# Kernel optimization log

Measured on AMD Instinct MI355X. Metric: run time of the kernel, lower is better.

The kernel has to match this reference:

```python
import jax, jax.numpy as jnp
import numpy as np

WINDOW = 60
DEPTH = 3
HIDDEN = 256
LN_EPS = 1e-5


def _lyndon_indices(d):
    # Lyndon words over alphabet {0..d-1}, lengths 2 and 3, lexicographic order
    # (signatory mode='words' extracts expanded-logsig coefficients at Lyndon words).
    i2 = np.array([(i, j) for i in range(d) for j in range(d) if (i, j) < (j, i)], dtype=np.int32)
    i3 = np.array([(i, j, k) for i in range(d) for j in range(d) for k in range(d)
                   if (i, j, k) < (j, k, i) and (i, j, k) < (k, i, j)], dtype=np.int32)
    return i2, i3


def _logsig_features(x):
    # x: [b, s, c] -> logsignature of time-augmented sliding windows: [b*s, sig_channels]
    b, s, c = x.shape
    d = c + 1
    # replicate-padded sliding windows via clipped gather (matches F.pad replicate + unfold)
    pos = jnp.clip(jnp.arange(s)[:, None] + jnp.arange(WINDOW)[None, :] - (WINDOW - 1), 0, s - 1)
    windows = x[:, pos, :]                                   # [b, s, W, c]
    t = jnp.linspace(0.0, 1.0, WINDOW, dtype=x.dtype)        # time augmentation channel
    t_b = jnp.broadcast_to(t[None, None, :, None], (b, s, WINDOW, 1))
    aug = jnp.concatenate([t_b, windows], axis=-1).reshape(b * s, WINDOW, d)
    N = b * s
    # basepoint=True: prepend zero point -> increments include the first point itself
    inc = jnp.diff(aug, axis=1, prepend=jnp.zeros((N, 1, d), aug.dtype))  # [N, W, d]
    inc_t = jnp.transpose(inc, (1, 0, 2))                    # [W, N, d]

    def chen_step(carry, v):
        S1, S2, S3 = carry
        vv = jnp.einsum('ni,nj->nij', v, v)
        vvv = jnp.einsum('nij,nk->nijk', vv, v)
        nS3 = S3 + jnp.einsum('nij,nk->nijk', S2, v) \
                 + 0.5 * jnp.einsum('ni,njk->nijk', S1, vv) + vvv / 6.0
        nS2 = S2 + jnp.einsum('ni,nj->nij', S1, v) + 0.5 * vv
        nS1 = S1 + v
        return (nS1, nS2, nS3), None

    init = (jnp.zeros((N, d), x.dtype), jnp.zeros((N, d, d), x.dtype), jnp.zeros((N, d, d, d), x.dtype))
    (S1, S2, S3), _ = jax.lax.scan(chen_step, init, inc_t)
    # log in truncated tensor algebra: log(1+x) = x - x^2/2 + x^3/3
    L1 = S1
    L2 = S2 - 0.5 * jnp.einsum('ni,nj->nij', S1, S1)
    L3 = (S3 - 0.5 * (jnp.einsum('ni,njk->nijk', S1, S2) + jnp.einsum('nij,nk->nijk', S2, S1))
          + jnp.einsum('ni,nj,nk->nijk', S1, S1, S1) / 3.0)
    i2, i3 = _lyndon_indices(d)
    f2 = L2[:, i2[:, 0], i2[:, 1]]
    f3 = L3[:, i3[:, 0], i3[:, 1], i3[:, 2]]
    return jnp.concatenate([L1, f2, f3], axis=-1)            # [N, sig_channels]


def setup_inputs() -> dict:
    key = jax.random.key(0)
    ks = jax.random.split(key, 5)
    b, s, c = 8, 2048, 8
    d = c + 1
    sig_channels = d + (d * d - d) // 2 + (d ** 3 - d) // 3  # 285 for d=9
    h2 = 2 * HIDDEN
    x = jax.random.normal(ks[0], (b, s, c), dtype=jnp.float32)
    w1 = jax.random.normal(ks[1], (sig_channels, h2), dtype=jnp.float32) / np.sqrt(sig_channels)
    b1 = jnp.zeros((h2,), jnp.float32)
    ln_g = jnp.ones((h2,), jnp.float32)
    ln_b = jnp.zeros((h2,), jnp.float32)
    w2 = jax.random.normal(ks[2], (h2, HIDDEN), dtype=jnp.float32) / np.sqrt(h2)
    b2 = jnp.zeros((HIDDEN,), jnp.float32)
    return {"x": x, "w1": w1, "b1": b1, "ln_g": ln_g, "ln_b": ln_b, "w2": w2, "b2": b2}


def reference(x, w1, b1, ln_g, ln_b, w2, b2):
    b, s, _ = x.shape
    feats = _logsig_features(x)                              # [b*s, sig_channels]
    h = jax.nn.gelu(feats @ w1 + b1, approximate=False)      # torch default GELU (erf)
    mu = jnp.mean(h, axis=-1, keepdims=True)
    var = jnp.var(h, axis=-1, keepdims=True)
    h = (h - mu) / jnp.sqrt(var + LN_EPS) * ln_g + ln_b      # LayerNorm; Dropout is eval no-op
    out = h @ w2 + b2
    return out.reshape(b, s, -1)
```

## Files before the change

kernel.cpp:

```cpp
#include <hip/hip_runtime.h>
#include <hip/hip_bf16.h>
#include <cstdint>
#include <cstddef>

typedef short short8 __attribute__((ext_vector_type(8)));
typedef float f32x4 __attribute__((ext_vector_type(4)));
typedef float f32x2 __attribute__((ext_vector_type(2)));

#define NS    2048
#define KPAD  288
#define H2    512
#define HID   256
#define WPB   7
#define SBLK  293

#define MFMA(a,b,c) __builtin_amdgcn_mfma_f32_16x16x32_bf16((a),(b),(c),0,0,0)

__device__ __forceinline__ void gl2lds16(const void* g, void* l) {
    __builtin_amdgcn_global_load_lds(
        (const __attribute__((address_space(1))) void*)g,
        (__attribute__((address_space(3))) void*)l, 16, 0, 0);
}
__device__ __forceinline__ float geluf(float x) {
    return 0.5f * x * (1.0f + erff(x * 0.70710678118654752f));
}
__device__ __forceinline__ f32x4 shfl4(f32x4 v, int d) {
    f32x4 r;
    r[0] = __shfl_xor(v[0], d); r[1] = __shfl_xor(v[1], d);
    r[2] = __shfl_xor(v[2], d); r[3] = __shfl_xor(v[3], d);
    return r;
}

struct Tbl3 { short col[729]; };
static constexpr Tbl3 make_tbl3() {
    Tbl3 t{};
    for (int x = 0; x < 729; ++x) t.col[x] = -1;
    int r = 0;
    for (int i = 0; i < 9; ++i)
        for (int j = 0; j < 9; ++j)
            for (int k = 0; k < 9; ++k) {
                bool lt1 = (i < j) || (i == j && (j < k || (j == k && k < i)));
                bool lt2 = (i < k) || (i == k && (j < i || (j == i && k < j)));
                if (lt1 && lt2) { t.col[(i*9+j)*9+k] = (short)(45 + r); ++r; }
            }
    return t;
}
static constexpr Tbl3 TBL3 = make_tbl3();

#define SIG_STEP(VA_,VB_,VC_) { \
    const float hh = 0.5f * S1i + vi * (1.0f/6.0f); \
    const float ra = S2ra + hh * (VA_); \
    const float rb = S2rb + hh * (VB_); \
    const float rc = S2rc + hh * (VC_); \
    const f32x2 ra2 = {ra, ra}, rb2 = {rb, rb}, rc2 = {rc, rc}; \
    S3sa += ra * v0; S3pa0 += ra2*vp0; S3pa1 += ra2*vp1; S3pa2 += ra2*vp2; S3pa3 += ra2*vp3; \
    S3sb += rb * v0; S3pb0 += rb2*vp0; S3pb1 += rb2*vp1; S3pb2 += rb2*vp2; S3pb3 += rb2*vp3; \
    S3sc += rc * v0; S3pc0 += rc2*vp0; S3pc1 += rc2*vp1; S3pc2 += rc2*vp2; S3pc3 += rc2*vp3; \
    const float aa = S1i + 0.5f * vi; \
    S2ra += aa * (VA_); S2rb += aa * (VB_); S2rc += aa * (VC_); \
    S1i += vi; }

#define SIG_MAIN(VA_,VB_,VC_) { \
    { const float* xr = &X[(g0 - lo) * 8]; \
      const float4 e0 = *(const float4*)xr; \
      const float4 e1 = *(const float4*)(xr + 4); \
      const float rs = xr[ioff]; \
      const float v0 = 0.0f; \
      const f32x2 vp0 = {e0.x, e0.y}, vp1 = {e0.z, e0.w}, vp2 = {e1.x, e1.y}, vp3 = {e1.z, e1.w}; \
      const float vi = (ci == 0) ? 0.0f : rs; \
      SIG_STEP(VA_,VB_,VC_) } \
    const float* pd = &PD[(sm59 + 1 - lo + 59) * 8]; \
    float4 d0 = *(const float4*)pd; \
    float4 d1 = *(const float4*)(pd + 4); \
    float rn = pd[ioff]; \
    _Pragma("unroll 2") \
    for (int j = 1; j < 60; ++j) { \
      const float4 e0 = d0; const float4 e1 = d1; const float rs = rn; \
      pd += 8; \
      d0 = *(const float4*)pd; d1 = *(const float4*)(pd + 4); rn = pd[ioff]; \
      const float v0 = DT; \
      const f32x2 vp0 = {e0.x, e0.y}, vp1 = {e0.z, e0.w}, vp2 = {e1.x, e1.y}, vp3 = {e1.z, e1.w}; \
      const float vi = (ci == 0) ? DT : rs; \
      SIG_STEP(VA_,VB_,VC_) \
    } }

#define SIG_ST(RA,RB,RC) \
    if (act) { \
        if ((RA) == 0) S1buf[widx * 9 + ci] = S1i; \
        float* sb = &S2buf[widx * 81 + ci * 9]; \
        sb[RA] = S2ra; sb[RB] = S2rb; sb[RC] = S2rc; \
    }

#define S3EL0(SL) S3s##SL
#define S3EL1(SL) S3p##SL##0[0]
#define S3EL2(SL) S3p##SL##0[1]
#define S3EL3(SL) S3p##SL##1[0]
#define S3EL4(SL) S3p##SL##1[1]
#define S3EL5(SL) S3p##SL##2[0]
#define S3EL6(SL) S3p##SL##2[1]
#define S3EL7(SL) S3p##SL##3[0]
#define S3EL8(SL) S3p##SL##3[1]

#define SIG_E2(SL,J2) if (ci < (J2)) { \
    const float val2 = S2r##SL - 0.5f * S1i * s1v##J2; \
    const int col2 = 9 + ci*8 - (ci*(ci-1))/2 + ((J2) - ci - 1); \
    frow[col2] = __float2bfloat16(val2); }

#define SIG_E3(SL,R,K) { const int col3 = TBL3.col[tb + (R)*9 + (K)]; \
    if (col3 >= 0) { \
        const float val3 = S3EL##K(SL) \
            - 0.5f * (S1i * S2w[(R)*9+(K)] + S2r##SL * s1v##K) \
            + S1i * s1v##R * s1v##K * (1.0f/3.0f); \
        frow[col3] = __float2bfloat16(val3); } }

#define SIG_E3R(SL,R) SIG_E3(SL,R,0) SIG_E3(SL,R,1) SIG_E3(SL,R,2) SIG_E3(SL,R,3) \
    SIG_E3(SL,R,4) SIG_E3(SL,R,5) SIG_E3(SL,R,6) SIG_E3(SL,R,7) SIG_E3(SL,R,8)

#define SIG_EMIT(RA,RB,RC) \
    if (act) { \
        if ((RA) == 0) { \
            frow[ci] = __float2bfloat16(S1i); \
            if (ci == 0) { \
                const __hip_bfloat16 z16 = __float2bfloat16(0.0f); \
                frow[285] = z16; frow[286] = z16; frow[287] = z16; \
            } \
        } \
        SIG_E2(a,RA) SIG_E2(b,RB) SIG_E2(c,RC) \
        SIG_E3R(a,RA) SIG_E3R(b,RB) SIG_E3R(c,RC) \
    }

__global__ __launch_bounds__(192) __attribute__((amdgpu_waves_per_eu(1, 6)))
void sig_kernel(const float* __restrict__ x, __hip_bfloat16* __restrict__ feats) {
    __shared__ __align__(16) float X[66 * 8];
    __shared__ __align__(16) float PD[126 * 8];
    __shared__ float S2buf[WPB * 81];
    __shared__ float S1buf[WPB * 9];

    const int blk = blockIdx.x;
    const int b   = blk / SBLK;
    const int s0  = (blk % SBLK) * WPB;
    const int lo  = (s0 - 59 > 0) ? (s0 - 59) : 0;
    const int hi  = (s0 + WPB - 1 < NS - 1) ? (s0 + WPB - 1) : (NS - 1);
    const int nrow = hi - lo + 1;
    const int tid = threadIdx.x;

    {
        const float4* src = (const float4*)(x + ((size_t)b * NS + lo) * 8);
        float4* X4 = (float4*)X;
        const int n4 = nrow * 2;
        for (int t = tid; t < n4; t += 192) X4[t] = src[t];
    }
    __syncthreads();
    {
        const float4* X4 = (const float4*)X;
        float4* PD4 = (float4*)PD;
        for (int t = tid; t < 252; t += 192) {
            const int p = t >> 1;
            const int r = p - 59;
            float4 dv = {0.f, 0.f, 0.f, 0.f};
            if (r > 0 && r < nrow) {
                const float4 a = X4[t - 118], bb = X4[t - 120];
                dv.x = a.x - bb.x; dv.y = a.y - bb.y; dv.z = a.z - bb.z; dv.w = a.w - bb.w;
            }
            PD4[t] = dv;
        }
    }
    __syncthreads();

    const int t3    = tid >> 6;
    const int lt    = tid & 63;
    const int widx0 = lt / 9;
    const int ci    = lt - widx0 * 9;
    const bool act  = (lt < 63) && (s0 + widx0 < NS);
    const int widx  = (widx0 < WPB - 1) ? widx0 : WPB - 1;
    int s = s0 + widx; if (s > NS - 1) s = NS - 1;

    float S3sa=0.f, S3sb=0.f, S3sc=0.f;
    f32x2 S3pa0={0.f,0.f},S3pa1={0.f,0.f},S3pa2={0.f,0.f},S3pa3={0.f,0.f};
    f32x2 S3pb0={0.f,0.f},S3pb1={0.f,0.f},S3pb2={0.f,0.f},S3pb3={0.f,0.f};
    f32x2 S3pc0={0.f,0.f},S3pc1={0.f,0.f},S3pc2={0.f,0.f},S3pc3={0.f,0.f};
    float S2ra=0.f, S2rb=0.f, S2rc=0.f;
    float S1i = 0.f;
    const int ioff = (ci > 0) ? (ci - 1) : 0;
    const int sm59 = s - 59;
    const int g0   = (sm59 > 0) ? sm59 : 0;
    const float DT = 1.0f / 59.0f;

    if (t3 == 0)      { SIG_MAIN(v0,   e0.x, e0.y) }
    else if (t3 == 1) { SIG_MAIN(e0.z, e0.w, e1.x) }
    else              { SIG_MAIN(e1.y, e1.z, e1.w) }

    if (t3 == 0)      { SIG_ST(0,1,2) }
    else if (t3 == 1) { SIG_ST(3,4,5) }
    else              { SIG_ST(6,7,8) }
    __syncthreads();

    const float* s1p = &S1buf[widx * 9];
    const float s1v0=s1p[0], s1v1=s1p[1], s1v2=s1p[2], s1v3=s1p[3], s1v4=s1p[4];
    const float s1v5=s1p[5], s1v6=s1p[6], s1v7=s1p[7], s1v8=s1p[8];
    const float* S2w = &S2buf[widx * 81];
    const int tb = ci * 81;
    __hip_bfloat16* frow = feats + (size_t)(b * NS + s) * KPAD;

    if (t3 == 0)      { SIG_EMIT(0,1,2) }
    else if (t3 == 1) { SIG_EMIT(3,4,5) }
    else              { SIG_EMIT(6,7,8) }
}

__global__ __launch_bounds__(512)
void prep_kernel(const float* __restrict__ w1, const float* __restrict__ w2,
                 const float* __restrict__ lng, const float* __restrict__ lnb,
                 const float* __restrict__ b2,
                 __hip_bfloat16* __restrict__ w1T, __hip_bfloat16* __restrict__ w2g,
                 float* __restrict__ gw, float* __restrict__ cvec,
                 float* __restrict__ stats) {
    const int blk = blockIdx.x;
    if (blk < 256) {
        const int n = blk, k = threadIdx.x;
        const float wv = w2[(size_t)k * HID + n];
        const float a = lng[k] * wv;
        const float c = lnb[k] * wv;
        w2g[(size_t)n * H2 + k] = __float2bfloat16(a);
        float ra = a, rc = c;
#pragma unroll
        for (int d = 1; d < 64; d <<= 1) { ra += __shfl_xor(ra, d); rc += __shfl_xor(rc, d); }
        __shared__ float r1[8], r2[8];
        const int wv_ = k >> 6, ln = k & 63;
        if (ln == 0) { r1[wv_] = ra; r2[wv_] = rc; }
        __syncthreads();
        if (k == 0) {
            float sa = 0.f, sc = 0.f;
#pragma unroll
            for (int i = 0; i < 8; ++i) { sa += r1[i]; sc += r2[i]; }
            gw[n] = sa; cvec[n] = sc + b2[n];
        }
    } else {
        const int n = blk - 256;
        const int k = threadIdx.x;
        if (k < KPAD) {
            const float v = (k < 285) ? w1[(size_t)k * H2 + n] : 0.0f;
            w1T[(size_t)n * KPAD + k] = __float2bfloat16(v);
        }
        if (k < 64) stats[n * 64 + k] = 0.0f;
    }
}

#define GDECL \
    f32x4 acc00={0,0,0,0},acc01={0,0,0,0},acc02={0,0,0,0},acc03={0,0,0,0}; \
    f32x4 acc10={0,0,0,0},acc11={0,0,0,0},acc12={0,0,0,0},acc13={0,0,0,0}; \
    f32x4 acc20={0,0,0,0},acc21={0,0,0,0},acc22={0,0,0,0},acc23={0,0,0,0}; \
    f32x4 acc30={0,0,0,0},acc31={0,0,0,0},acc32={0,0,0,0},acc33={0,0,0,0};

#define GMROW(mf) { const short8 av = *(const short8*)(abase + (mf)*512); \
    acc##mf##0 = MFMA(av, b0v, acc##mf##0); acc##mf##1 = MFMA(av, b1v, acc##mf##1); \
    acc##mf##2 = MFMA(av, b2v, acc##mf##2); acc##mf##3 = MFMA(av, b3v, acc##mf##3); }

#define GSTAGE(APTR, BPTR, KD, K0, LA, LB) { \
    int c = tid; \
    gl2lds16((APTR) + (size_t)(m0 + (c>>2))*(KD) + (K0) + (c&3)*8, (char*)(LA) + (c & ~63)*16); \
    gl2lds16((BPTR) + (size_t)(n0 + (c>>2))*(KD) + (K0) + (c&3)*8, (char*)(LB) + (c & ~63)*16); \
    c = tid + 256; \
    gl2lds16((APTR) + (size_t)(m0 + (c>>2))*(KD) + (K0) + (c&3)*8, (char*)(LA) + (c & ~63)*16); \
    gl2lds16((BPTR) + (size_t)(n0 + (c>>2))*(KD) + (K0) + (c&3)*8, (char*)(LB) + (c & ~63)*16); }

#define GCOMP(LA, LB) { \
    const __hip_bfloat16* abase = (LA) + (mh + l16)*32 + quad*8; \
    const __hip_bfloat16* bbase = (LB) + (nh + l16)*32 + quad*8; \
    const short8 b0v = *(const short8*)(bbase); \
    const short8 b1v = *(const short8*)(bbase + 512); \
    const short8 b2v = *(const short8*)(bbase + 1024); \
    const short8 b3v = *(const short8*)(bbase + 1536); \
    GMROW(0) GMROW(1) GMROW(2) GMROW(3) }

#define GEMM_PIPE(APTR, BPTR, KD, KSTEPS) \
    GSTAGE(APTR, BPTR, KD, 0, ldsA0, ldsB0) \
    __syncthreads(); \
    _Pragma("unroll 1") \
    for (int kt = 0; kt < (KSTEPS); kt += 2) { \
        if (kt + 1 < (KSTEPS)) { GSTAGE(APTR, BPTR, KD, (kt+1)*32, ldsA1, ldsB1) } \
        GCOMP(ldsA0, ldsB0) \
        __syncthreads(); \
        if (kt + 1 < (KSTEPS)) { \
            if (kt + 2 < (KSTEPS)) { GSTAGE(APTR, BPTR, KD, (kt+2)*32, ldsA0, ldsB0) } \
            GCOMP(ldsA1, ldsB1) \
            __syncthreads(); \
        } \
    }

#define G1EP(mf,nf) { \
    const int colv = n0 + nh + (nf)*16 + l16; \
    const float bv = bias[colv]; \
    f32x4 e; \
    e[0] = geluf(acc##mf##nf[0] + bv); e[1] = geluf(acc##mf##nf[1] + bv); \
    e[2] = geluf(acc##mf##nf[2] + bv); e[3] = geluf(acc##mf##nf[3] + bv); \
    const int rrow = m0 + mh + (mf)*16 + quad*4; \
    h1[(size_t)(rrow+0)*H2 + colv] = __float2bfloat16(e[0]); \
    h1[(size_t)(rrow+1)*H2 + colv] = __float2bfloat16(e[1]); \
    h1[(size_t)(rrow+2)*H2 + colv] = __float2bfloat16(e[2]); \
    h1[(size_t)(rrow+3)*H2 + colv] = __float2bfloat16(e[3]); \
    sum##mf += e; sq##mf += e*e; }

#define G1RED(mf) { \
    f32x4 s = sum##mf, q = sq##mf; \
    s += shfl4(s,1); q += shfl4(q,1); s += shfl4(s,2); q += shfl4(q,2); \
    s += shfl4(s,4); q += shfl4(q,4); s += shfl4(s,8); q += shfl4(q,8); \
    if (l16 == 0) { const int rrow = m0 + mh + (mf)*16 + quad*4; \
        atomicAdd(&stats[2*(rrow+0)],   s[0]); atomicAdd(&stats[2*(rrow+0)+1], q[0]); \
        atomicAdd(&stats[2*(rrow+1)],   s[1]); atomicAdd(&stats[2*(rrow+1)+1], q[1]); \
        atomicAdd(&stats[2*(rrow+2)],   s[2]); atomicAdd(&stats[2*(rrow+2)+1], q[2]); \
        atomicAdd(&stats[2*(rrow+3)],   s[3]); atomicAdd(&stats[2*(rrow+3)+1], q[3]); } }

__global__ __launch_bounds__(256) __attribute__((amdgpu_waves_per_eu(1, 4)))
void gemm1_kernel(const __hip_bfloat16* __restrict__ feats,
                  const __hip_bfloat16* __restrict__ w1T,
                  const float* __restrict__ bias,
                  __hip_bfloat16* __restrict__ h1,
                  float* __restrict__ stats) {
    __shared__ __align__(16) __hip_bfloat16 ldsA0[128 * 32];
    __shared__ __align__(16) __hip_bfloat16 ldsB0[128 * 32];
    __shared__ __align__(16) __hip_bfloat16 ldsA1[128 * 32];
    __shared__ __align__(16) __hip_bfloat16 ldsB1[128 * 32];
    const int tid  = threadIdx.x;
    const int wave = tid >> 6;
    const int lane = tid & 63;
    const int quad = lane >> 4;
    const int l16  = lane & 15;
    const int mh   = (wave >> 1) * 64;
    const int nh   = (wave & 1) * 64;
    const int m0   = blockIdx.x * 128;
    const int n0   = blockIdx.y * 128;
    GDECL
    GEMM_PIPE(feats, w1T, KPAD, 9)
    f32x4 sum0={0,0,0,0},sum1={0,0,0,0},sum2={0,0,0,0},sum3={0,0,0,0};
    f32x4 sq0={0,0,0,0},sq1={0,0,0,0},sq2={0,0,0,0},sq3={0,0,0,0};
    G1EP(0,0) G1EP(0,1) G1EP(0,2) G1EP(0,3)
    G1EP(1,0) G1EP(1,1) G1EP(1,2) G1EP(1,3)
    G1EP(2,0) G1EP(2,1) G1EP(2,2) G1EP(2,3)
    G1EP(3,0) G1EP(3,1) G1EP(3,2) G1EP(3,3)
    G1RED(0) G1RED(1) G1RED(2) G1RED(3)
}

#define STATR(r) { const float su = stats[2*(rrow+(r))]; const float qu = stats[2*(rrow+(r))+1]; \
    const float m_ = su * (1.0f/512.0f); const float v_ = qu * (1.0f/512.0f) - m_*m_; \
    muv[r] = m_; rsv[r] = rsqrtf(v_ + 1e-5f); }

#define G2C(mf,nf) { const int colv = n0 + nh + (nf)*16 + l16; \
    const float g_ = gw[colv], c_ = cvec[colv]; \
    out[(size_t)(rrow+0)*HID + colv] = rsv[0]*(acc##mf##nf[0] - muv[0]*g_) + c_; \
    out[(size_t)(rrow+1)*HID + colv] = rsv[1]*(acc##mf##nf[1] - muv[1]*g_) + c_; \
    out[(size_t)(rrow+2)*HID + colv] = rsv[2]*(acc##mf##nf[2] - muv[2]*g_) + c_; \
    out[(size_t)(rrow+3)*HID + colv] = rsv[3]*(acc##mf##nf[3] - muv[3]*g_) + c_; }

#define G2EP(mf) { const int rrow = m0 + mh + (mf)*16 + quad*4; \
    f32x4 muv, rsv; \
    STATR(0) STATR(1) STATR(2) STATR(3) \
    G2C(mf,0) G2C(mf,1) G2C(mf,2) G2C(mf,3) }

__global__ __launch_bounds__(256) __attribute__((amdgpu_waves_per_eu(1, 4)))
void gemm2_kernel(const __hip_bfloat16* __restrict__ h1,
                  const __hip_bfloat16* __restrict__ w2g,
                  const float* __restrict__ stats,
                  const float* __restrict__ gw,
                  const float* __restrict__ cvec,
                  float* __restrict__ out) {
    __shared__ __align__(16) __hip_bfloat16 ldsA0[128 * 32];
    __shared__ __align__(16) __hip_bfloat16 ldsB0[128 * 32];
    __shared__ __align__(16) __hip_bfloat16 ldsA1[128 * 32];
    __shared__ __align__(16) __hip_bfloat16 ldsB1[128 * 32];
    const int tid  = threadIdx.x;
    const int wave = tid >> 6;
    const int lane = tid & 63;
    const int quad = lane >> 4;
    const int l16  = lane & 15;
    const int mh   = (wave >> 1) * 64;
    const int nh   = (wave & 1) * 64;
    const int m0   = blockIdx.x * 128;
    const int n0   = blockIdx.y * 128;
    GDECL
    GEMM_PIPE(h1, w2g, H2, 16)
    G2EP(0) G2EP(1) G2EP(2) G2EP(3)
}

extern "C" void kernel_launch(void* const* d_in, const int* in_sizes, int n_in,
                              void* d_out, int out_size, void* d_ws, size_t ws_size,
                              hipStream_t stream) {
    const float* x   = (const float*)d_in[0];
    const float* w1  = (const float*)d_in[1];
    const float* b1  = (const float*)d_in[2];
    const float* lng = (const float*)d_in[3];
    const float* lnb = (const float*)d_in[4];
    const float* w2  = (const float*)d_in[5];
    const float* b2  = (const float*)d_in[6];
    float* out = (float*)d_out;

    char* ws = (char*)d_ws;
    __hip_bfloat16* feats = (__hip_bfloat16*)(ws);
    __hip_bfloat16* h1    = (__hip_bfloat16*)(ws + 9437184);
    __hip_bfloat16* w1T   = (__hip_bfloat16*)(ws + 26214400);
    __hip_bfloat16* w2g   = (__hip_bfloat16*)(ws + 26509312);
    float*          gw    = (float*)(ws + 26771456);
    float*          cvec  = (float*)(ws + 26775552);
    float*          stats = (float*)(ws + 26779648);

    prep_kernel<<<dim3(768), dim3(512), 0, stream>>>(w1, w2, lng, lnb, b2,
                                                     w1T, w2g, gw, cvec, stats);
    sig_kernel<<<dim3(8 * SBLK), dim3(192), 0, stream>>>(x, feats);
    gemm1_kernel<<<dim3(128, 4), dim3(256), 0, stream>>>(feats, w1T, b1, h1, stats);
    gemm2_kernel<<<dim3(128, 2), dim3(256), 0, stream>>>(h1, w2g, stats, gw, cvec, out);
}
```

Baseline: 155.5 us.

## Retile both GEMMs to 64x64 blocks with XOR-swizzled LDS layouts

Both GEMMs move from 128x128 to 64x64 output tiles, giving four times as many blocks. gemm1 now loads the whole K=288 slab into LDS in one pass and drops the double-buffered loop. gemm2 uses 128-wide K stages, double buffered. LDS rows are XOR-swizzled to cut bank conflicts, and w1T is padded to a 320-element row stride. The aim is better CU occupancy and less pipeline overhead; in exchange, operand reuse per block drops and the stats atomics increase.

```diff
diff --git a/kernel.cpp b/kernel.cpp
--- a/kernel.cpp
+++ b/kernel.cpp
@@ -237,69 +237,76 @@
     } else {
         const int n = blk - 256;
         const int k = threadIdx.x;
-        if (k < KPAD) {
+        if (k < 320) {
             const float v = (k < 285) ? w1[(size_t)k * H2 + n] : 0.0f;
-            w1T[(size_t)n * KPAD + k] = __float2bfloat16(v);
+            w1T[(size_t)n * 320 + k] = __float2bfloat16(v);
         }
         if (k < 64) stats[n * 64 + k] = 0.0f;
     }
 }
 
-#define GDECL \
-    f32x4 acc00={0,0,0,0},acc01={0,0,0,0},acc02={0,0,0,0},acc03={0,0,0,0}; \
-    f32x4 acc10={0,0,0,0},acc11={0,0,0,0},acc12={0,0,0,0},acc13={0,0,0,0}; \
-    f32x4 acc20={0,0,0,0},acc21={0,0,0,0},acc22={0,0,0,0},acc23={0,0,0,0}; \
-    f32x4 acc30={0,0,0,0},acc31={0,0,0,0},acc32={0,0,0,0},acc33={0,0,0,0};
-
-#define GMROW(mf) { const short8 av = *(const short8*)(abase + (mf)*512); \
-    acc##mf##0 = MFMA(av, b0v, acc##mf##0); acc##mf##1 = MFMA(av, b1v, acc##mf##1); \
-    acc##mf##2 = MFMA(av, b2v, acc##mf##2); acc##mf##3 = MFMA(av, b3v, acc##mf##3); }
-
-#define GSTAGE(APTR, BPTR, KD, K0, LA, LB) { \
-    int c = tid; \
-    gl2lds16((APTR) + (size_t)(m0 + (c>>2))*(KD) + (K0) + (c&3)*8, (char*)(LA) + (c & ~63)*16); \
-    gl2lds16((BPTR) + (size_t)(n0 + (c>>2))*(KD) + (K0) + (c&3)*8, (char*)(LB) + (c & ~63)*16); \
-    c = tid + 256; \
-    gl2lds16((APTR) + (size_t)(m0 + (c>>2))*(KD) + (K0) + (c&3)*8, (char*)(LA) + (c & ~63)*16); \
-    gl2lds16((BPTR) + (size_t)(n0 + (c>>2))*(KD) + (K0) + (c&3)*8, (char*)(LB) + (c & ~63)*16); }
-
-#define GCOMP(LA, LB) { \
-    const __hip_bfloat16* abase = (LA) + (mh + l16)*32 + quad*8; \
-    const __hip_bfloat16* bbase = (LB) + (nh + l16)*32 + quad*8; \
-    const short8 b0v = *(const short8*)(bbase); \
-    const short8 b1v = *(const short8*)(bbase + 512); \
-    const short8 b2v = *(const short8*)(bbase + 1024); \
-    const short8 b3v = *(const short8*)(bbase + 1536); \
-    GMROW(0) GMROW(1) GMROW(2) GMROW(3) }
-
-#define GEMM_PIPE(APTR, BPTR, KD, KSTEPS) \
-    GSTAGE(APTR, BPTR, KD, 0, ldsA0, ldsB0) \
-    __syncthreads(); \
-    _Pragma("unroll 1") \
-    for (int kt = 0; kt < (KSTEPS); kt += 2) { \
-        if (kt + 1 < (KSTEPS)) { GSTAGE(APTR, BPTR, KD, (kt+1)*32, ldsA1, ldsB1) } \
-        GCOMP(ldsA0, ldsB0) \
-        __syncthreads(); \
-        if (kt + 1 < (KSTEPS)) { \
-            if (kt + 2 < (KSTEPS)) { GSTAGE(APTR, BPTR, KD, (kt+2)*32, ldsA0, ldsB0) } \
-            GCOMP(ldsA1, ldsB1) \
-            __syncthreads(); \
-        } \
-    }
-
-#define G1EP(mf,nf) { \
+__global__ __launch_bounds__(256)
+void gemm1_kernel(const __hip_bfloat16* __restrict__ feats,
+                  const __hip_bfloat16* __restrict__ w1T,
+                  const float* __restrict__ bias,
+                  __hip_bfloat16* __restrict__ h1,
+                  float* __restrict__ stats) {
+    __shared__ __align__(16) __hip_bfloat16 ldsA[64 * 320];
+    __shared__ __align__(16) __hip_bfloat16 ldsB[64 * 320];
+    const int tid  = threadIdx.x;
+    const int wave = tid >> 6;
+    const int lane = tid & 63;
+    const int quad = lane >> 4;
+    const int l16  = lane & 15;
+    const int mh   = (wave >> 1) * 32;
+    const int nh   = (wave & 1) * 32;
+    const int n0   = blockIdx.x * 64;
+    const int m0   = blockIdx.y * 64;
+
+    const char* Ab = (const char*)feats;
+    const char* Bb = (const char*)w1T;
+#pragma unroll
+    for (int t = 0; t < 10; ++t) {
+        const int L   = tid + t * 256;
+        const int row = L / 40;
+        const int blk = L - row * 40;
+        const int sb  = (blk ^ (row & 7)) * 16;
+        gl2lds16(Ab + (size_t)(m0 + row) * 576 + sb, (char*)ldsA + (L & ~63) * 16);
+        gl2lds16(Bb + (size_t)(n0 + row) * 640 + sb, (char*)ldsB + (L & ~63) * 16);
+    }
+    __syncthreads();
+
+    f32x4 acc00={0,0,0,0}, acc01={0,0,0,0}, acc10={0,0,0,0}, acc11={0,0,0,0};
+    const int x0 = (l16 & 7) << 4;
+    const char* A0 = (const char*)ldsA + (mh + l16) * 640;
+    const char* A1 = A0 + 16 * 640;
+    const char* B0 = (const char*)ldsB + (nh + l16) * 640;
+    const char* B1 = B0 + 16 * 640;
+#pragma unroll
+    for (int kt = 0; kt < 9; ++kt) {
+        const int ka = (kt * 64 + quad * 16) ^ x0;
+        const short8 a0 = *(const short8*)(A0 + ka);
+        const short8 a1 = *(const short8*)(A1 + ka);
+        const short8 b0 = *(const short8*)(B0 + ka);
+        const short8 b1 = *(const short8*)(B1 + ka);
+        acc00 = MFMA(a0, b0, acc00); acc01 = MFMA(a0, b1, acc01);
+        acc10 = MFMA(a1, b0, acc10); acc11 = MFMA(a1, b1, acc11);
+    }
+
+    f32x4 sum0={0,0,0,0}, sum1={0,0,0,0}, sq0={0,0,0,0}, sq1={0,0,0,0};
+#define G1EP(mf,nf,ACC) { \
     const int colv = n0 + nh + (nf)*16 + l16; \
     const float bv = bias[colv]; \
     f32x4 e; \
-    e[0] = geluf(acc##mf##nf[0] + bv); e[1] = geluf(acc##mf##nf[1] + bv); \
-    e[2] = geluf(acc##mf##nf[2] + bv); e[3] = geluf(acc##mf##nf[3] + bv); \
+    e[0] = geluf(ACC[0] + bv); e[1] = geluf(ACC[1] + bv); \
+    e[2] = geluf(ACC[2] + bv); e[3] = geluf(ACC[3] + bv); \
     const int rrow = m0 + mh + (mf)*16 + quad*4; \
     h1[(size_t)(rrow+0)*H2 + colv] = __float2bfloat16(e[0]); \
     h1[(size_t)(rrow+1)*H2 + colv] = __float2bfloat16(e[1]); \
     h1[(size_t)(rrow+2)*H2 + colv] = __float2bfloat16(e[2]); \
     h1[(size_t)(rrow+3)*H2 + colv] = __float2bfloat16(e[3]); \
     sum##mf += e; sq##mf += e*e; }
-
+    G1EP(0,0,acc00) G1EP(0,1,acc01) G1EP(1,0,acc10) G1EP(1,1,acc11)
 #define G1RED(mf) { \
     f32x4 s = sum##mf, q = sq##mf; \
     s += shfl4(s,1); q += shfl4(q,1); s += shfl4(s,2); q += shfl4(q,2); \
@@ -309,76 +316,92 @@
         atomicAdd(&stats[2*(rrow+1)],   s[1]); atomicAdd(&stats[2*(rrow+1)+1], q[1]); \
         atomicAdd(&stats[2*(rrow+2)],   s[2]); atomicAdd(&stats[2*(rrow+2)+1], q[2]); \
         atomicAdd(&stats[2*(rrow+3)],   s[3]); atomicAdd(&stats[2*(rrow+3)+1], q[3]); } }
-
-__global__ __launch_bounds__(256) __attribute__((amdgpu_waves_per_eu(1, 4)))
-void gemm1_kernel(const __hip_bfloat16* __restrict__ feats,
-                  const __hip_bfloat16* __restrict__ w1T,
-                  const float* __restrict__ bias,
-                  __hip_bfloat16* __restrict__ h1,
-                  float* __restrict__ stats) {
-    __shared__ __align__(16) __hip_bfloat16 ldsA0[128 * 32];
-    __shared__ __align__(16) __hip_bfloat16 ldsB0[128 * 32];
-    __shared__ __align__(16) __hip_bfloat16 ldsA1[128 * 32];
-    __shared__ __align__(16) __hip_bfloat16 ldsB1[128 * 32];
-    const int tid  = threadIdx.x;
-    const int wave = tid >> 6;
-    const int lane = tid & 63;
-    const int quad = lane >> 4;
-    const int l16  = lane & 15;
-    const int mh   = (wave >> 1) * 64;
-    const int nh   = (wave & 1) * 64;
-    const int m0   = blockIdx.x * 128;
-    const int n0   = blockIdx.y * 128;
-    GDECL
-    GEMM_PIPE(feats, w1T, KPAD, 9)
-    f32x4 sum0={0,0,0,0},sum1={0,0,0,0},sum2={0,0,0,0},sum3={0,0,0,0};
-    f32x4 sq0={0,0,0,0},sq1={0,0,0,0},sq2={0,0,0,0},sq3={0,0,0,0};
-    G1EP(0,0) G1EP(0,1) G1EP(0,2) G1EP(0,3)
-    G1EP(1,0) G1EP(1,1) G1EP(1,2) G1EP(1,3)
-    G1EP(2,0) G1EP(2,1) G1EP(2,2) G1EP(2,3)
-    G1EP(3,0) G1EP(3,1) G1EP(3,2) G1EP(3,3)
-    G1RED(0) G1RED(1) G1RED(2) G1RED(3)
-}
-
-#define STATR(r) { const float su = stats[2*(rrow+(r))]; const float qu = stats[2*(rrow+(r))+1]; \
-    const float m_ = su * (1.0f/512.0f); const float v_ = qu * (1.0f/512.0f) - m_*m_; \
-    muv[r] = m_; rsv[r] = rsqrtf(v_ + 1e-5f); }
-
-#define G2C(mf,nf) { const int colv = n0 + nh + (nf)*16 + l16; \
-    const float g_ = gw[colv], c_ = cvec[colv]; \
-    out[(size_t)(rrow+0)*HID + colv] = rsv[0]*(acc##mf##nf[0] - muv[0]*g_) + c_; \
-    out[(size_t)(rrow+1)*HID + colv] = rsv[1]*(acc##mf##nf[1] - muv[1]*g_) + c_; \
-    out[(size_t)(rrow+2)*HID + colv] = rsv[2]*(acc##mf##nf[2] - muv[2]*g_) + c_; \
-    out[(size_t)(rrow+3)*HID + colv] = rsv[3]*(acc##mf##nf[3] - muv[3]*g_) + c_; }
-
-#define G2EP(mf) { const int rrow = m0 + mh + (mf)*16 + quad*4; \
-    f32x4 muv, rsv; \
-    STATR(0) STATR(1) STATR(2) STATR(3) \
-    G2C(mf,0) G2C(mf,1) G2C(mf,2) G2C(mf,3) }
-
-__global__ __launch_bounds__(256) __attribute__((amdgpu_waves_per_eu(1, 4)))
+    G1RED(0) G1RED(1)
+}
+
+__global__ __launch_bounds__(256)
 void gemm2_kernel(const __hip_bfloat16* __restrict__ h1,
                   const __hip_bfloat16* __restrict__ w2g,
                   const float* __restrict__ stats,
                   const float* __restrict__ gw,
                   const float* __restrict__ cvec,
                   float* __restrict__ out) {
-    __shared__ __align__(16) __hip_bfloat16 ldsA0[128 * 32];
-    __shared__ __align__(16) __hip_bfloat16 ldsB0[128 * 32];
-    __shared__ __align__(16) __hip_bfloat16 ldsA1[128 * 32];
-    __shared__ __align__(16) __hip_bfloat16 ldsB1[128 * 32];
+    __shared__ __align__(16) __hip_bfloat16 ldsA[2][64 * 128];
+    __shared__ __align__(16) __hip_bfloat16 ldsB[2][64 * 128];
     const int tid  = threadIdx.x;
     const int wave = tid >> 6;
     const int lane = tid & 63;
     const int quad = lane >> 4;
     const int l16  = lane & 15;
-    const int mh   = (wave >> 1) * 64;
-    const int nh   = (wave & 1) * 64;
-    const int m0   = blockIdx.x * 128;
-    const int n0   = blockIdx.y * 128;
-    GDECL
-    GEMM_PIPE(h1, w2g, H2, 16)
-    G2EP(0) G2EP(1) G2EP(2) G2EP(3)
+    const int mh   = (wave >> 1) * 32;
+    const int nh   = (wave & 1) * 32;
+    const int n0   = blockIdx.x * 64;
+    const int m0   = blockIdx.y * 64;
+
+    const char* Ab = (const char*)h1;
+    const char* Bb = (const char*)w2g;
+
+#define G2STAGE(S, BUF) { \
+    _Pragma("unroll") \
+    for (int t = 0; t < 4; ++t) { \
+        const int L   = tid + t * 256;      \
+        const int row = L >> 4; \
+        const int blk = L & 15; \
+        const int sb  = (S) * 256 + ((blk ^ (row & 7)) * 16); \
+        gl2lds16(Ab + (size_t)(m0 + row) * 1024 + sb, (char*)ldsA[BUF] + (L & ~63) * 16); \
+        gl2lds16(Bb + (size_t)(n0 + row) * 1024 + sb, (char*)ldsB[BUF] + (L & ~63) * 16); \
+    } }
+
+    f32x4 acc00={0,0,0,0}, acc01={0,0,0,0}, acc10={0,0,0,0}, acc11={0,0,0,0};
+    const int x0 = (l16 & 7) << 4;
+
+#define G2COMP(BUF) { \
+    const char* A0 = (const char*)ldsA[BUF] + (mh + l16) * 256; \
+    const char* A1 = A0 + 16 * 256; \
+    const char* B0 = (const char*)ldsB[BUF] + (nh + l16) * 256; \
+    const char* B1 = B0 + 16 * 256; \
+    _Pragma("unroll") \
+    for (int kt = 0; kt < 4; ++kt) { \
+        const int ka = (kt * 64 + quad * 16) ^ x0; \
+        const short8 a0 = *(const short8*)(A0 + ka); \
+        const short8 a1 = *(const short8*)(A1 + ka); \
+        const short8 b0 = *(const short8*)(B0 + ka); \
+        const short8 b1 = *(const short8*)(B1 + ka); \
+        acc00 = MFMA(a0, b0, acc00); acc01 = MFMA(a0, b1, acc01); \
+        acc10 = MFMA(a1, b0, acc10); acc11 = MFMA(a1, b1, acc11); \
+    } }
+
+    G2STAGE(0, 0)
+    __syncthreads();
+#pragma unroll 1
+    for (int s = 0; s < 4; ++s) {
+        if (s < 3) { G2STAGE(s + 1, (s + 1) & 1) }
+        G2COMP(s & 1)
+        __syncthreads();
+    }
+
+#define G2EP(mf, ACC0, ACC1) { \
+    const int rrow = m0 + mh + (mf)*16 + quad*4; \
+    f32x4 muv, rsv; \
+    _Pragma("unroll") \
+    for (int r = 0; r < 4; ++r) { \
+        const float su = stats[2*(rrow+r)]; const float qu = stats[2*(rrow+r)+1]; \
+        const float m_ = su * (1.0f/512.0f); const float v_ = qu * (1.0f/512.0f) - m_*m_; \
+        muv[r] = m_; rsv[r] = rsqrtf(v_ + 1e-5f); } \
+    { const int colv = n0 + nh + l16; \
+      const float g_ = gw[colv], c_ = cvec[colv]; \
+      out[(size_t)(rrow+0)*HID + colv] = rsv[0]*(ACC0[0] - muv[0]*g_) + c_; \
+      out[(size_t)(rrow+1)*HID + colv] = rsv[1]*(ACC0[1] - muv[1]*g_) + c_; \
+      out[(size_t)(rrow+2)*HID + colv] = rsv[2]*(ACC0[2] - muv[2]*g_) + c_; \
+      out[(size_t)(rrow+3)*HID + colv] = rsv[3]*(ACC0[3] - muv[3]*g_) + c_; } \
+    { const int colv = n0 + nh + 16 + l16; \
+      const float g_ = gw[colv], c_ = cvec[colv]; \
+      out[(size_t)(rrow+0)*HID + colv] = rsv[0]*(ACC1[0] - muv[0]*g_) + c_; \
+      out[(size_t)(rrow+1)*HID + colv] = rsv[1]*(ACC1[1] - muv[1]*g_) + c_; \
+      out[(size_t)(rrow+2)*HID + colv] = rsv[2]*(ACC1[2] - muv[2]*g_) + c_; \
+      out[(size_t)(rrow+3)*HID + colv] = rsv[3]*(ACC1[3] - muv[3]*g_) + c_; } }
+    G2EP(0, acc00, acc01)
+    G2EP(1, acc10, acc11)
 }
 
 extern "C" void kernel_launch(void* const* d_in, const int* in_sizes, int n_in,
@@ -397,14 +420,14 @@
     __hip_bfloat16* feats = (__hip_bfloat16*)(ws);
     __hip_bfloat16* h1    = (__hip_bfloat16*)(ws + 9437184);
     __hip_bfloat16* w1T   = (__hip_bfloat16*)(ws + 26214400);
-    __hip_bfloat16* w2g   = (__hip_bfloat16*)(ws + 26509312);
-    float*          gw    = (float*)(ws + 26771456);
-    float*          cvec  = (float*)(ws + 26775552);
-    float*          stats = (float*)(ws + 26779648);
+    __hip_bfloat16* w2g   = (__hip_bfloat16*)(ws + 26542080);
+    float*          gw    = (float*)(ws + 26804224);
+    float*          cvec  = (float*)(ws + 26808320);
+    float*          stats = (float*)(ws + 26812416);
 
     prep_kernel<<<dim3(768), dim3(512), 0, stream>>>(w1, w2, lng, lnb, b2,
                                                      w1T, w2g, gw, cvec, stats);
     sig_kernel<<<dim3(8 * SBLK), dim3(192), 0, stream>>>(x, feats);
-    gemm1_kernel<<<dim3(128, 4), dim3(256), 0, stream>>>(feats, w1T, b1, h1, stats);
-    gemm2_kernel<<<dim3(128, 2), dim3(256), 0, stream>>>(h1, w2g, stats, gw, cvec, out);
-}
+    gemm1_kernel<<<dim3(8, 256), dim3(256), 0, stream>>>(feats, w1T, b1, h1, stats);
+    gemm2_kernel<<<dim3(4, 256), dim3(256), 0, stream>>>(h1, w2g, stats, gw, cvec, out);
+}
```

Result: slower. 169.5 us (+9.0%).

## Split signature window scan into two halves combined via Chen's identity

Applied to the files above, without the earlier changes.

Doubles the signature kernel block to 384 threads. Each window's 60-step sequential Chen recursion is split into two halves computed by separate wave groups, and the second half's S1/S2/S3 are merged into the first via Chen's product identity through LDS. This halves the serial dependency chain per thread to raise parallelism. In exchange it adds about 23KB of LDS per block for the S3 exchange, an extra barrier, and combine arithmetic, which may reduce occupancy.

```diff
diff --git a/kernel.cpp b/kernel.cpp
--- a/kernel.cpp
+++ b/kernel.cpp
@@ -30,6 +30,7 @@
     r[2] = __shfl_xor(v[2], d); r[3] = __shfl_xor(v[3], d);
     return r;
 }
+__device__ __forceinline__ f32x2 mk2(float a, float b) { f32x2 r; r[0] = a; r[1] = b; return r; }
 
 struct Tbl3 { short col[729]; };
 static constexpr Tbl3 make_tbl3() {
@@ -60,7 +61,22 @@
     S2ra += aa * (VA_); S2rb += aa * (VB_); S2rc += aa * (VC_); \
     S1i += vi; }
 
-#define SIG_MAIN(VA_,VB_,VC_) { \
+#define SIG_DIFFS(NITER, VA_,VB_,VC_) { \
+    float4 d0 = *(const float4*)pd; \
+    float4 d1 = *(const float4*)(pd + 4); \
+    float rn = pd[ioff]; \
+    _Pragma("unroll 2") \
+    for (int j = 0; j < (NITER); ++j) { \
+      const float4 e0 = d0; const float4 e1 = d1; const float rs = rn; \
+      pd += 8; \
+      d0 = *(const float4*)pd; d1 = *(const float4*)(pd + 4); rn = pd[ioff]; \
+      const float v0 = DT; \
+      const f32x2 vp0 = {e0.x, e0.y}, vp1 = {e0.z, e0.w}, vp2 = {e1.x, e1.y}, vp3 = {e1.z, e1.w}; \
+      const float vi = (ci == 0) ? DT : rs; \
+      SIG_STEP(VA_,VB_,VC_) \
+    } }
+
+#define SIG_MAIN_A(VA_,VB_,VC_) { \
     { const float* xr = &X[(g0 - lo) * 8]; \
       const float4 e0 = *(const float4*)xr; \
       const float4 e1 = *(const float4*)(xr + 4); \
@@ -70,26 +86,54 @@
       const float vi = (ci == 0) ? 0.0f : rs; \
       SIG_STEP(VA_,VB_,VC_) } \
     const float* pd = &PD[(sm59 + 1 - lo + 59) * 8]; \
-    float4 d0 = *(const float4*)pd; \
-    float4 d1 = *(const float4*)(pd + 4); \
-    float rn = pd[ioff]; \
-    _Pragma("unroll 2") \
-    for (int j = 1; j < 60; ++j) { \
-      const float4 e0 = d0; const float4 e1 = d1; const float rs = rn; \
-      pd += 8; \
-      d0 = *(const float4*)pd; d1 = *(const float4*)(pd + 4); rn = pd[ioff]; \
-      const float v0 = DT; \
-      const f32x2 vp0 = {e0.x, e0.y}, vp1 = {e0.z, e0.w}, vp2 = {e1.x, e1.y}, vp3 = {e1.z, e1.w}; \
-      const float vi = (ci == 0) ? DT : rs; \
-      SIG_STEP(VA_,VB_,VC_) \
+    SIG_DIFFS(29, VA_,VB_,VC_) }
+
+#define SIG_MAIN_B(VA_,VB_,VC_) { \
+    const float* pd = &PD[(sm59 + 30 - lo + 59) * 8]; \
+    SIG_DIFFS(30, VA_,VB_,VC_) }
+
+#define SIG_STB(RA,RB,RC) \
+    if (act) { \
+        if ((RA) == 0) S1B[widx * 9 + ci] = S1i; \
+        float* sb = &S2B[widx * 81 + ci * 9]; \
+        sb[RA] = S2ra; sb[RB] = S2rb; sb[RC] = S2rc; \
+        float* s3 = &S3B[widx * 810 + ci * 90]; \
+        s3[(RA)*10] = S3sa; *(f32x2*)(s3+(RA)*10+2) = S3pa0; *(f32x2*)(s3+(RA)*10+4) = S3pa1; \
+        *(f32x2*)(s3+(RA)*10+6) = S3pa2; *(f32x2*)(s3+(RA)*10+8) = S3pa3; \
+        s3[(RB)*10] = S3sb; *(f32x2*)(s3+(RB)*10+2) = S3pb0; *(f32x2*)(s3+(RB)*10+4) = S3pb1; \
+        *(f32x2*)(s3+(RB)*10+6) = S3pb2; *(f32x2*)(s3+(RB)*10+8) = S3pb3; \
+        s3[(RC)*10] = S3sc; *(f32x2*)(s3+(RC)*10+2) = S3pc0; *(f32x2*)(s3+(RC)*10+4) = S3pc1; \
+        *(f32x2*)(s3+(RC)*10+6) = S3pc2; *(f32x2*)(s3+(RC)*10+8) = S3pc3; \
+    }
+
+#define SIG_CMB(SL,R) { \
+    const float* bb  = s3b + (R)*10; \
+    const float* s2r = s2b + (R)*9; \
+    const f32x2 sr2 = {S2r##SL, S2r##SL}; \
+    S3s##SL   += bb[0] + S1i * s2r[0] + S2r##SL * s1b[0]; \
+    S3p##SL##0 += *(const f32x2*)(bb+2) + s1i2*mk2(s2r[1],s2r[2]) + sr2*sbp0; \
+    S3p##SL##1 += *(const f32x2*)(bb+4) + s1i2*mk2(s2r[3],s2r[4]) + sr2*sbp1; \
+    S3p##SL##2 += *(const f32x2*)(bb+6) + s1i2*mk2(s2r[5],s2r[6]) + sr2*sbp2; \
+    S3p##SL##3 += *(const f32x2*)(bb+8) + s1i2*mk2(s2r[7],s2r[8]) + sr2*sbp3; }
+
+#define SIG_COMBINE(RA,RB,RC) { \
+    const float* s1b = &S1B[widx * 9]; \
+    const float* s2b = &S2B[widx * 81]; \
+    const float* s3b = &S3B[widx * 810 + ci * 90]; \
+    const f32x2 s1i2 = {S1i, S1i}; \
+    const f32x2 sbp0 = mk2(s1b[1], s1b[2]), sbp1 = mk2(s1b[3], s1b[4]); \
+    const f32x2 sbp2 = mk2(s1b[5], s1b[6]), sbp3 = mk2(s1b[7], s1b[8]); \
+    SIG_CMB(a,RA) SIG_CMB(b,RB) SIG_CMB(c,RC) \
+    const float nS2a = S2ra + s2b[ci*9+(RA)] + S1i * s1b[RA]; \
+    const float nS2b = S2rb + s2b[ci*9+(RB)] + S1i * s1b[RB]; \
+    const float nS2c = S2rc + s2b[ci*9+(RC)] + S1i * s1b[RC]; \
+    S2ra = nS2a; S2rb = nS2b; S2rc = nS2c; \
+    S1i += s1b[ci]; \
+    if (act) { \
+        if ((RA) == 0) S1F[widx * 9 + ci] = S1i; \
+        float* sf = &S2F[widx * 81 + ci * 9]; \
+        sf[RA] = S2ra; sf[RB] = S2rb; sf[RC] = S2rc; \
     } }
-
-#define SIG_ST(RA,RB,RC) \
-    if (act) { \
-        if ((RA) == 0) S1buf[widx * 9 + ci] = S1i; \
-        float* sb = &S2buf[widx * 81 + ci * 9]; \
-        sb[RA] = S2ra; sb[RB] = S2rb; sb[RC] = S2rc; \
-    }
 
 #define S3EL0(SL) S3s##SL
 #define S3EL1(SL) S3p##SL##0[0]
@@ -129,12 +173,15 @@
         SIG_E3R(a,RA) SIG_E3R(b,RB) SIG_E3R(c,RC) \
     }
 
-__global__ __launch_bounds__(192) __attribute__((amdgpu_waves_per_eu(1, 6)))
+__global__ __launch_bounds__(384)
 void sig_kernel(const float* __restrict__ x, __hip_bfloat16* __restrict__ feats) {
     __shared__ __align__(16) float X[66 * 8];
     __shared__ __align__(16) float PD[126 * 8];
-    __shared__ float S2buf[WPB * 81];
-    __shared__ float S1buf[WPB * 9];
+    __shared__ float S2B[WPB * 81];
+    __shared__ float S1B[WPB * 9];
+    __shared__ float S2F[WPB * 81];
+    __shared__ float S1F[WPB * 9];
+    __shared__ __align__(16) float S3B[WPB * 810];
 
     const int blk = blockIdx.x;
     const int b   = blk / SBLK;
@@ -148,13 +195,13 @@
         const float4* src = (const float4*)(x + ((size_t)b * NS + lo) * 8);
         float4* X4 = (float4*)X;
         const int n4 = nrow * 2;
-        for (int t = tid; t < n4; t += 192) X4[t] = src[t];
+        for (int t = tid; t < n4; t += 384) X4[t] = src[t];
     }
     __syncthreads();
     {
         const float4* X4 = (const float4*)X;
         float4* PD4 = (float4*)PD;
-        for (int t = tid; t < 252; t += 192) {
+        for (int t = tid; t < 252; t += 384) {
             const int p = t >> 1;
             const int r = p - 59;
             float4 dv = {0.f, 0.f, 0.f, 0.f};
@@ -167,7 +214,9 @@
     }
     __syncthreads();
 
-    const int t3    = tid >> 6;
+    const int wav   = tid >> 6;
+    const int hB    = (wav >= 3);
+    const int t3    = hB ? (wav - 3) : wav;
     const int lt    = tid & 63;
     const int widx0 = lt / 9;
     const int ci    = lt - widx0 * 9;
@@ -186,25 +235,39 @@
     const int g0   = (sm59 > 0) ? sm59 : 0;
     const float DT = 1.0f / 59.0f;
 
-    if (t3 == 0)      { SIG_MAIN(v0,   e0.x, e0.y) }
-    else if (t3 == 1) { SIG_MAIN(e0.z, e0.w, e1.x) }
-    else              { SIG_MAIN(e1.y, e1.z, e1.w) }
-
-    if (t3 == 0)      { SIG_ST(0,1,2) }
-    else if (t3 == 1) { SIG_ST(3,4,5) }
-    else              { SIG_ST(6,7,8) }
+    if (!hB) {
+        if (t3 == 0)      { SIG_MAIN_A(v0,   e0.x, e0.y) }
+        else if (t3 == 1) { SIG_MAIN_A(e0.z, e0.w, e1.x) }
+        else              { SIG_MAIN_A(e1.y, e1.z, e1.w) }
+    } else {
+        if (t3 == 0)      { SIG_MAIN_B(v0,   e0.x, e0.y) }
+        else if (t3 == 1) { SIG_MAIN_B(e0.z, e0.w, e1.x) }
+        else              { SIG_MAIN_B(e1.y, e1.z, e1.w) }
+        if (t3 == 0)      { SIG_STB(0,1,2) }
+        else if (t3 == 1) { SIG_STB(3,4,5) }
+        else              { SIG_STB(6,7,8) }
+    }
     __syncthreads();
 
-    const float* s1p = &S1buf[widx * 9];
-    const float s1v0=s1p[0], s1v1=s1p[1], s1v2=s1p[2], s1v3=s1p[3], s1v4=s1p[4];
-    const float s1v5=s1p[5], s1v6=s1p[6], s1v7=s1p[7], s1v8=s1p[8];
-    const float* S2w = &S2buf[widx * 81];
-    const int tb = ci * 81;
-    __hip_bfloat16* frow = feats + (size_t)(b * NS + s) * KPAD;
-
-    if (t3 == 0)      { SIG_EMIT(0,1,2) }
-    else if (t3 == 1) { SIG_EMIT(3,4,5) }
-    else              { SIG_EMIT(6,7,8) }
+    if (!hB) {
+        if (t3 == 0)      { SIG_COMBINE(0,1,2) }
+        else if (t3 == 1) { SIG_COMBINE(3,4,5) }
+        else              { SIG_COMBINE(6,7,8) }
+    }
+    __syncthreads();
+
+    if (!hB) {
+        const float* s1p = &S1F[widx * 9];
+        const float s1v0=s1p[0], s1v1=s1p[1], s1v2=s1p[2], s1v3=s1p[3], s1v4=s1p[4];
+        const float s1v5=s1p[5], s1v6=s1p[6], s1v7=s1p[7], s1v8=s1p[8];
+        const float* S2w = &S2F[widx * 81];
+        const int tb = ci * 81;
+        __hip_bfloat16* frow = feats + (size_t)(b * NS + s) * KPAD;
+
+        if (t3 == 0)      { SIG_EMIT(0,1,2) }
+        else if (t3 == 1) { SIG_EMIT(3,4,5) }
+        else              { SIG_EMIT(6,7,8) }
+    }
 }
 
 __global__ __launch_bounds__(512)
@@ -404,7 +467,7 @@
 
     prep_kernel<<<dim3(768), dim3(512), 0, stream>>>(w1, w2, lng, lnb, b2,
                                                      w1T, w2g, gw, cvec, stats);
-    sig_kernel<<<dim3(8 * SBLK), dim3(192), 0, stream>>>(x, feats);
+    sig_kernel<<<dim3(8 * SBLK), dim3(384), 0, stream>>>(x, feats);
     gemm1_kernel<<<dim3(128, 4), dim3(256), 0, stream>>>(feats, w1T, b1, h1, stats);
     gemm2_kernel<<<dim3(128, 2), dim3(256), 0, stream>>>(h1, w2g, stats, gw, cvec, out);
 }
```

Result: slower. 168.7 us (+8.5%).
